# Performance work log

Hardware: AMD Instinct MI355X
Metric: run time of the kernel (lower is better)

Reference implementation:

```python
import jax, jax.numpy as jnp
import numpy as np

MAX_LENGTH = 256
WIDTH = 4


def _attention_matrix(a, b):
    # a, b: (B, M, D) with M = max_length + width - 1
    # euclidean match score: 1 / (1 + ||a_i - b_j||_2)
    sq = (
        jnp.sum(a * a, axis=-1)[:, :, None]
        + jnp.sum(b * b, axis=-1)[:, None, :]
        - 2.0 * jnp.einsum('bid,bjd->bij', a, b)
    )
    dist = jnp.sqrt(jnp.maximum(sq, 0.0))
    return 1.0 / (1.0 + dist)  # (B, M, M)


def reference(x1, x2):
    # x1, x2: (B, 1, M, D), M = MAX_LENGTH + WIDTH - 1
    a = x1[:, 0]  # (B, M, D)
    b = x2[:, 0]
    A = _attention_matrix(a, b)  # (B, M, M), A[b,i,j] = score(a_i, b_j)
    # row_sum over dim i of A[:,:,k] weights x1 column k; col analogously for x2.
    w_a = jnp.sum(A, axis=1)  # (B, M): sum_i A[i, k]
    w_b = jnp.sum(A, axis=2)  # (B, M): sum_j A[k, j]
    y1 = w_a[:, :, None] * a  # (B, M, D)
    y2 = w_b[:, :, None] * b
    # sliding-window sum of width WIDTH: w[j] = sum_{k=j}^{j+WIDTH-1} y[k]
    w1 = sum(y1[:, d:d + MAX_LENGTH, :] for d in range(WIDTH))
    w2 = sum(y2[:, d:d + MAX_LENGTH, :] for d in range(WIDTH))
    return (w1[:, None], w2[:, None])  # (B, 1, MAX_LENGTH, D) each


def setup_inputs() -> dict:
    key = jax.random.key(0)
    k1, k2 = jax.random.split(key)
    B, M, D = 128, MAX_LENGTH + WIDTH - 1, 512
    x1 = jax.random.normal(k1, (B, 1, M, D), dtype=jnp.float32)
    x2 = jax.random.normal(k2, (B, 1, M, D), dtype=jnp.float32)
    return {"x1": x1, "x2": x2}
```

## Files before the change

kernel.cpp:

```cpp
#include <hip/hip_runtime.h>

#define BATCH 128
#define M 259
#define D 512
#define T 256
#define NM (BATCH * M)
#define OUTHALF (BATCH * T * D)
#define MP 320
#define HJ 160
#define PROWS 480
#define BK 64

typedef __bf16 bf16;
typedef __bf16 bf16x4 __attribute__((ext_vector_type(4)));
typedef __bf16 bf16x8 __attribute__((ext_vector_type(8)));
typedef float f32x4 __attribute__((ext_vector_type(4)));


__global__ void k_zero(float* __restrict__ ws) {
    int i = blockIdx.x * 256 + threadIdx.x;
    if (i < NM) ws[NM + i] = 0.f;
}

__launch_bounds__(512)
__global__ void k_pairs(const float* __restrict__ x1, const float* __restrict__ x2,
                        float* __restrict__ ws) {
    __shared__ __align__(16) bf16 P[PROWS * BK];
    __shared__ float nrm[PROWS];
    __shared__ float wcol_s[HJ];

    int sblk = blockIdx.x;
    int bid  = (sblk & 7) * 32 + (sblk >> 3);
    int b  = bid >> 1;
    int jh = bid & 1;
    int j0 = jh * 130;

    int t    = threadIdx.x;
    int lane = t & 63;
    int w    = t >> 6;
    int wm   = w >> 1;
    int wn   = w & 1;

    const float* Ab = x1 + (size_t)b * M * D;
    const float* Bb = x2 + (size_t)b * M * D;

    if (t < HJ) wcol_s[t] = 0.f;

    int q = t >> 4, c4f = t & 15;
    int off[15], wro[15];
#pragma unroll
    for (int p = 0; p < 15; ++p) {
        int row  = q + 32 * p;
        int grow = (p < 10) ? min(row, M - 1) : min(j0 + (row - MP), M - 1);
        off[p] = grow * D + c4f * 4;
        wro[p] = row * BK + (((c4f >> 1) ^ (row & 7)) << 3) + (t & 1) * 4;
    }

    int a_off[5][2], b_off[5][2];
#pragma unroll
    for (int f = 0; f < 5; ++f) {
        int rowa = wm * 80 + f * 16 + (lane & 15);
        int rowb = MP + wn * 80 + f * 16 + (lane & 15);
#pragma unroll
        for (int kk = 0; kk < 2; ++kk) {
            int slot = kk * 4 + (lane >> 4);
            a_off[f][kk] = rowa * BK + ((slot ^ (rowa & 7)) << 3);
            b_off[f][kk] = rowb * BK + ((slot ^ (rowb & 7)) << 3);
        }
    }

    f32x4 acc[5][5];
#pragma unroll
    for (int fi = 0; fi < 5; ++fi)
#pragma unroll
        for (int fj = 0; fj < 5; ++fj) acc[fi][fj] = (f32x4)0.f;

    float sa[15];
#pragma unroll
    for (int p = 0; p < 15; ++p) sa[p] = 0.f;

#define STAGE5(P0, BASE) do {                                                   \
        float4 v_[5];                                                           \
        _Pragma("unroll")                                                       \
        for (int i_ = 0; i_ < 5; ++i_)                                          \
            v_[i_] = *(const float4*)((BASE) + off[(P0) + i_] + k0);            \
        _Pragma("unroll")                                                       \
        for (int i_ = 0; i_ < 5; ++i_) {                                        \
            sa[(P0) + i_] += v_[i_].x * v_[i_].x + v_[i_].y * v_[i_].y          \
                           + v_[i_].z * v_[i_].z + v_[i_].w * v_[i_].w;         \
            *(bf16x4*)&P[wro[(P0) + i_]] = bf16x4{ (bf16)v_[i_].x,              \
                (bf16)v_[i_].y, (bf16)v_[i_].z, (bf16)v_[i_].w };               \
        } } while (0)

    for (int k0 = 0; k0 < D; k0 += BK) {
        __syncthreads();
        STAGE5(0, Ab);
        STAGE5(5, Ab);
        STAGE5(10, Bb);
        __syncthreads();
#pragma unroll
        for (int kk = 0; kk < 2; ++kk) {
            bf16x8 af[5], bfr[5];
#pragma unroll
            for (int f = 0; f < 5; ++f) af[f]  = *(const bf16x8*)&P[a_off[f][kk]];
#pragma unroll
            for (int f = 0; f < 5; ++f) bfr[f] = *(const bf16x8*)&P[b_off[f][kk]];
#pragma unroll
            for (int fi = 0; fi < 5; ++fi)
#pragma unroll
                for (int fj = 0; fj < 5; ++fj)
                    acc[fi][fj] = __builtin_amdgcn_mfma_f32_16x16x32_bf16(
                        af[fi], bfr[fj], acc[fi][fj], 0, 0, 0);
        }
    }
#undef STAGE5

#pragma unroll
    for (int p = 0; p < 15; ++p) {
        float v = sa[p];
        v += __shfl_xor(v, 1); v += __shfl_xor(v, 2);
        v += __shfl_xor(v, 4); v += __shfl_xor(v, 8);
        if ((t & 15) == 0) nrm[q + 32 * p] = v;
    }
    __syncthreads();

    float na_[5][4], nb_[5];
#pragma unroll
    for (int f = 0; f < 5; ++f) {
#pragma unroll
        for (int r = 0; r < 4; ++r)
            na_[f][r] = nrm[wm * 80 + f * 16 + (lane >> 4) * 4 + r];
        nb_[f] = nrm[MP + wn * 80 + f * 16 + (lane & 15)];
    }

    float rs[5][4], cs[5];
#pragma unroll
    for (int f = 0; f < 5; ++f) {
#pragma unroll
        for (int r = 0; r < 4; ++r) rs[f][r] = 0.f;
        cs[f] = 0.f;
    }

#pragma unroll
    for (int fi = 0; fi < 5; ++fi) {
#pragma unroll
        for (int fj = 0; fj < 5; ++fj) {
#pragma unroll
            for (int r = 0; r < 4; ++r) {
                int i  = wm * 80 + fi * 16 + (lane >> 4) * 4 + r;
                int lj = wn * 80 + fj * 16 + (lane & 15);
                int jg = j0 + lj;
                float av = 0.f;
                if (i < M && lj < 130 && jg < M) {
                    float sq   = na_[fi][r] + nb_[fj] - 2.f * acc[fi][fj][r];
                    float dist = sqrtf(fmaxf(sq, 0.f));
                    av = 1.f / (1.f + dist);
                }
                rs[fi][r] += av;
                cs[fj]    += av;
            }
        }
    }

    int b_off_w = b * M;
#pragma unroll
    for (int f = 0; f < 5; ++f)
#pragma unroll
        for (int r = 0; r < 4; ++r) {
            float v = rs[f][r];
            v += __shfl_xor(v, 1); v += __shfl_xor(v, 2);
            v += __shfl_xor(v, 4); v += __shfl_xor(v, 8);
            int i = wm * 80 + f * 16 + (lane >> 4) * 4 + r;
            if ((lane & 15) == 0 && i < M) atomicAdd(&ws[NM + b_off_w + i], v);
        }
#pragma unroll
    for (int f = 0; f < 5; ++f) {
        float v = cs[f];
        v += __shfl_xor(v, 16); v += __shfl_xor(v, 32);
        if ((lane >> 4) == 0)
            atomicAdd(&wcol_s[wn * 80 + f * 16 + (lane & 15)], v);
    }
    __syncthreads();
    if (t < HJ && t < 130 && j0 + t < M) ws[b_off_w + j0 + t] = wcol_s[t];
}

__global__ void k_out(const float* __restrict__ x1, const float* __restrict__ x2,
                      const float* __restrict__ ws, float* __restrict__ out) {
    int bid   = blockIdx.x;
    int which = bid & 1;
    int tc    = (bid >> 1) & 7;
    int b     = bid >> 4;
    int d4    = threadIdx.x << 2;
    const float* src  = which ? x2 : x1;
    const float* wgt  = ws + (which ? NM : 0) + b * M;
    const float* rows = src + (size_t)b * M * D + d4;
    float* o = out + (size_t)which * OUTHALF + ((size_t)b * T + tc * 32) * D + d4;
    int t0 = tc * 32;
    float4 v0 = *(const float4*)(rows + (size_t)(t0 + 0) * D);
    float4 v1 = *(const float4*)(rows + (size_t)(t0 + 1) * D);
    float4 v2 = *(const float4*)(rows + (size_t)(t0 + 2) * D);
    float s0 = wgt[t0 + 0], s1 = wgt[t0 + 1], s2 = wgt[t0 + 2];
#pragma unroll 4
    for (int tt = 0; tt < 32; ++tt) {
        float4 v3 = *(const float4*)(rows + (size_t)(t0 + tt + 3) * D);
        float s3  = wgt[t0 + tt + 3];
        float4 r;
        r.x = s0 * v0.x + s1 * v1.x + s2 * v2.x + s3 * v3.x;
        r.y = s0 * v0.y + s1 * v1.y + s2 * v2.y + s3 * v3.y;
        r.z = s0 * v0.z + s1 * v1.z + s2 * v2.z + s3 * v3.z;
        r.w = s0 * v0.w + s1 * v1.w + s2 * v2.w + s3 * v3.w;
        *(float4*)(o + (size_t)tt * D) = r;
        v0 = v1; v1 = v2; v2 = v3;
        s0 = s1; s1 = s2; s2 = s3;
    }
}

extern "C" void kernel_launch(void* const* d_in, const int* in_sizes, int n_in,
                              void* d_out, int out_size, void* d_ws, size_t ws_size,
                              hipStream_t stream) {
    const float* x1 = (const float*)d_in[0];
    const float* x2 = (const float*)d_in[1];
    float* out = (float*)d_out;
    float* ws  = (float*)d_ws;

    k_zero<<<(NM + 255) / 256, 256, 0, stream>>>(ws);
    k_pairs<<<256, 512, 0, stream>>>(x1, x2, ws);
    k_out<<<BATCH * 16, 128, 0, stream>>>(x1, x2, ws, out);
}
```

Measured before the change: 103.8 us.

## Split pairwise tile into 2x2 quadrants with smaller blocks and global atomics

The pairwise-distance kernel now tiles each batch into four 130x130 quadrants, giving 512 blocks of 256 threads instead of 256 blocks of 512 threads that each covered all rows against half the columns. Shared memory per block shrinks, and column sums go straight to global memory with atomics, which removes the shared column buffer and its barrier. The zeroing kernel now clears both weight arrays using float4 stores. In exchange, each A tile is staged twice across blocks, and global atomic traffic doubles.

After: 136.2 us. 1.31x slower.

```diff
diff --git a/kernel.cpp b/kernel.cpp
--- a/kernel.cpp
+++ b/kernel.cpp
@@ -6,9 +6,9 @@
 #define T 256
 #define NM (BATCH * M)
 #define OUTHALF (BATCH * T * D)
-#define MP 320
-#define HJ 160
-#define PROWS 480
+#define HB 130
+#define PAD 160
+#define PR 320
 #define BK 64
 
 typedef __bf16 bf16;
@@ -17,41 +17,40 @@
 typedef float f32x4 __attribute__((ext_vector_type(4)));
 
 
-__global__ void k_zero(float* __restrict__ ws) {
+__global__ void k_zero(float4* __restrict__ ws4) {
     int i = blockIdx.x * 256 + threadIdx.x;
-    if (i < NM) ws[NM + i] = 0.f;
-}
-
-__launch_bounds__(512)
+    if (i < (2 * NM + 3) / 4) ws4[i] = make_float4(0.f, 0.f, 0.f, 0.f);
+}
+
+__launch_bounds__(256)
 __global__ void k_pairs(const float* __restrict__ x1, const float* __restrict__ x2,
                         float* __restrict__ ws) {
-    __shared__ __align__(16) bf16 P[PROWS * BK];
-    __shared__ float nrm[PROWS];
-    __shared__ float wcol_s[HJ];
-
-    int sblk = blockIdx.x;
-    int bid  = (sblk & 7) * 32 + (sblk >> 3);
-    int b  = bid >> 1;
-    int jh = bid & 1;
-    int j0 = jh * 130;
+    __shared__ __align__(16) bf16 P[PR * BK];
+    __shared__ float nrm[PR];
+
+    int s   = blockIdx.x;
+    int bid = (s & 7) * 64 + (s >> 3);
+    int b   = bid >> 2;
+    int ih  = (bid >> 1) & 1;
+    int jh  = bid & 1;
+    int i0  = ih * HB;
+    int j0  = jh * HB;
 
     int t    = threadIdx.x;
     int lane = t & 63;
     int w    = t >> 6;
-    int wm   = w >> 1;
-    int wn   = w & 1;
+    int wm   = w >> 1, wn = w & 1;
 
     const float* Ab = x1 + (size_t)b * M * D;
     const float* Bb = x2 + (size_t)b * M * D;
 
-    if (t < HJ) wcol_s[t] = 0.f;
-
     int q = t >> 4, c4f = t & 15;
-    int off[15], wro[15];
-#pragma unroll
-    for (int p = 0; p < 15; ++p) {
-        int row  = q + 32 * p;
-        int grow = (p < 10) ? min(row, M - 1) : min(j0 + (row - MP), M - 1);
+    int off[20], wro[20];
+#pragma unroll
+    for (int p = 0; p < 20; ++p) {
+        int row  = q + 16 * p;
+        int grow = (p < 10) ? min(i0 + row, M - 1)
+                            : min(j0 + (row - PAD), M - 1);
         off[p] = grow * D + c4f * 4;
         wro[p] = row * BK + (((c4f >> 1) ^ (row & 7)) << 3) + (t & 1) * 4;
     }
@@ -60,7 +59,7 @@
 #pragma unroll
     for (int f = 0; f < 5; ++f) {
         int rowa = wm * 80 + f * 16 + (lane & 15);
-        int rowb = MP + wn * 80 + f * 16 + (lane & 15);
+        int rowb = PAD + wn * 80 + f * 16 + (lane & 15);
 #pragma unroll
         for (int kk = 0; kk < 2; ++kk) {
             int slot = kk * 4 + (lane >> 4);
@@ -75,9 +74,9 @@
 #pragma unroll
         for (int fj = 0; fj < 5; ++fj) acc[fi][fj] = (f32x4)0.f;
 
-    float sa[15];
-#pragma unroll
-    for (int p = 0; p < 15; ++p) sa[p] = 0.f;
+    float sa[20];
+#pragma unroll
+    for (int p = 0; p < 20; ++p) sa[p] = 0.f;
 
 #define STAGE5(P0, BASE) do {                                                   \
         float4 v_[5];                                                           \
@@ -94,9 +93,10 @@
 
     for (int k0 = 0; k0 < D; k0 += BK) {
         __syncthreads();
-        STAGE5(0, Ab);
-        STAGE5(5, Ab);
+        STAGE5(0,  Ab);
+        STAGE5(5,  Ab);
         STAGE5(10, Bb);
+        STAGE5(15, Bb);
         __syncthreads();
 #pragma unroll
         for (int kk = 0; kk < 2; ++kk) {
@@ -116,11 +116,11 @@
 #undef STAGE5
 
 #pragma unroll
-    for (int p = 0; p < 15; ++p) {
+    for (int p = 0; p < 20; ++p) {
         float v = sa[p];
         v += __shfl_xor(v, 1); v += __shfl_xor(v, 2);
         v += __shfl_xor(v, 4); v += __shfl_xor(v, 8);
-        if ((t & 15) == 0) nrm[q + 32 * p] = v;
+        if ((t & 15) == 0) nrm[q + 16 * p] = v;
     }
     __syncthreads();
 
@@ -130,7 +130,7 @@
 #pragma unroll
         for (int r = 0; r < 4; ++r)
             na_[f][r] = nrm[wm * 80 + f * 16 + (lane >> 4) * 4 + r];
-        nb_[f] = nrm[MP + wn * 80 + f * 16 + (lane & 15)];
+        nb_[f] = nrm[PAD + wn * 80 + f * 16 + (lane & 15)];
     }
 
     float rs[5][4], cs[5];
@@ -147,11 +147,11 @@
         for (int fj = 0; fj < 5; ++fj) {
 #pragma unroll
             for (int r = 0; r < 4; ++r) {
-                int i  = wm * 80 + fi * 16 + (lane >> 4) * 4 + r;
-                int lj = wn * 80 + fj * 16 + (lane & 15);
-                int jg = j0 + lj;
+                int il = wm * 80 + fi * 16 + (lane >> 4) * 4 + r;
+                int jl = wn * 80 + fj * 16 + (lane & 15);
+                int ig = i0 + il, jg = j0 + jl;
                 float av = 0.f;
-                if (i < M && lj < 130 && jg < M) {
+                if (il < HB && ig < M && jl < HB && jg < M) {
                     float sq   = na_[fi][r] + nb_[fj] - 2.f * acc[fi][fj][r];
                     float dist = sqrtf(fmaxf(sq, 0.f));
                     av = 1.f / (1.f + dist);
@@ -170,18 +170,20 @@
             float v = rs[f][r];
             v += __shfl_xor(v, 1); v += __shfl_xor(v, 2);
             v += __shfl_xor(v, 4); v += __shfl_xor(v, 8);
-            int i = wm * 80 + f * 16 + (lane >> 4) * 4 + r;
-            if ((lane & 15) == 0 && i < M) atomicAdd(&ws[NM + b_off_w + i], v);
+            int il = wm * 80 + f * 16 + (lane >> 4) * 4 + r;
+            int ig = i0 + il;
+            if ((lane & 15) == 0 && il < HB && ig < M)
+                atomicAdd(&ws[NM + b_off_w + ig], v);
         }
 #pragma unroll
     for (int f = 0; f < 5; ++f) {
         float v = cs[f];
         v += __shfl_xor(v, 16); v += __shfl_xor(v, 32);
-        if ((lane >> 4) == 0)
-            atomicAdd(&wcol_s[wn * 80 + f * 16 + (lane & 15)], v);
-    }
-    __syncthreads();
-    if (t < HJ && t < 130 && j0 + t < M) ws[b_off_w + j0 + t] = wcol_s[t];
+        int jl = wn * 80 + f * 16 + (lane & 15);
+        int jg = j0 + jl;
+        if ((lane >> 4) == 0 && jl < HB && jg < M)
+            atomicAdd(&ws[b_off_w + jg], v);
+    }
 }
 
 __global__ void k_out(const float* __restrict__ x1, const float* __restrict__ x2,
@@ -223,7 +225,7 @@
     float* out = (float*)d_out;
     float* ws  = (float*)d_ws;
 
-    k_zero<<<(NM + 255) / 256, 256, 0, stream>>>(ws);
-    k_pairs<<<256, 512, 0, stream>>>(x1, x2, ws);
+    k_zero<<<(2 * NM / 4 + 255) / 256, 256, 0, stream>>>((float4*)ws);
+    k_pairs<<<512, 256, 0, stream>>>(x1, x2, ws);
     k_out<<<BATCH * 16, 128, 0, stream>>>(x1, x2, ws, out);
 }
```
